# Kernel optimization log

Hardware: AMD Instinct MI355X
Metric: run time of the kernel (lower is better)

## Reference

```python
import jax, jax.numpy as jnp
import numpy as np

N = 100000      # nodes
E = 1200000     # edges (before self-loops)
DIN = 64        # n_input
DH = 64         # n_hidden
DOUT = 40       # n_output (classes)
L = 2           # n_layers
K = 4           # n_heads
ALPHA = 0.2
EPS = 1e-5


def setup_inputs() -> dict:
    key = jax.random.key(0)
    ks = jax.random.split(key, 12)
    s = lambda k, shape: jax.random.normal(k, shape, jnp.float32) * 0.05
    return {
        "x": jax.random.normal(ks[0], (N, DIN), jnp.float32),
        "edge_index": jax.random.randint(ks[1], (2, E), 0, N),
        # GCNConv weights: per layer l, per head k. conv_h: hidden->hidden, conv_x: input->hidden
        "Wh": s(ks[2], (L, K, DH, DH)), "bh": jnp.zeros((L, K, DH), jnp.float32),
        "Wx": s(ks[3], (L, K, DIN, DH)), "bx": jnp.zeros((L, K, DH), jnp.float32),
        # shared GatedModule
        "gf_w": s(ks[4], (2 * DH, 1)), "gf_b": jnp.zeros((1,), jnp.float32),
        "gu_w": s(ks[5], (2 * DH, 1)), "gu_b": jnp.zeros((1,), jnp.float32),
        # per-block FF
        "ff1_w": s(ks[6], (L, DH, DH)), "ff1_b": jnp.zeros((L, DH), jnp.float32),
        "ff2_w": s(ks[7], (L, DH, DH)), "ff2_b": jnp.zeros((L, DH), jnp.float32),
        # classifier head
        "clf1_w": s(ks[8], (DH, DH)), "clf1_b": jnp.zeros((DH,), jnp.float32),
        "clf2_w": s(ks[9], (DH, DOUT)), "clf2_b": jnp.zeros((DOUT,), jnp.float32),
    }


def _layer_norm(h):
    mu = jnp.mean(h, axis=-1, keepdims=True)
    var = jnp.mean((h - mu) ** 2, axis=-1, keepdims=True)
    return (h - mu) * jax.lax.rsqrt(var + EPS)


def reference(x, edge_index, Wh, bh, Wx, bx, gf_w, gf_b, gu_w, gu_b,
              ff1_w, ff1_b, ff2_w, ff2_b, clf1_w, clf1_b, clf2_w, clf2_b):
    # GCN normalization with self-loops: D^-1/2 (A+I) D^-1/2
    loops = jnp.arange(N)
    src = jnp.concatenate([edge_index[0], loops])  # [E+N]
    dst = jnp.concatenate([edge_index[1], loops])
    deg = jax.ops.segment_sum(jnp.ones_like(src, jnp.float32), dst, num_segments=N)
    dinv = jnp.where(deg > 0, jax.lax.rsqrt(jnp.maximum(deg, 1e-12)), 0.0)
    norm = dinv[src] * dinv[dst]  # [E+N] edge coefficients (shared by all convs)

    def gcn_conv(feat, W, b):
        m = feat @ W                                    # [N, DH] transform first (cheaper)
        agg = jax.ops.segment_sum(m[src] * norm[:, None], dst, num_segments=N)
        return agg + b

    def gate(h, xg):
        g = jnp.concatenate([h, xg], axis=1)            # [N, 2*DH]
        f = ALPHA * jnp.tanh(g @ gf_w + gf_b)
        u = ALPHA * jnp.tanh(g @ gu_w + gu_b)
        return (1.0 + f) * h + (1.0 + u) * xg

    h = jnp.zeros((N, DH), x.dtype)  # h0 = zeros (dropout is identity in eval mode)
    for l in range(L):
        acc = jnp.zeros((N, DH), x.dtype)
        for k in range(K):
            hk = gcn_conv(h, Wh[l, k], bh[l, k])
            xk = gcn_conv(x, Wx[l, k], bx[l, k])
            acc = acc + gate(hk, xk)
        h = acc / K + h                                  # multi-head mean + residual
        h = _layer_norm(h)
        ff = jax.nn.relu(h @ ff1_w[l] + ff1_b[l]) @ ff2_w[l] + ff2_b[l]
        h = _layer_norm(ff + h)
    return jax.nn.relu(h @ clf1_w + clf1_b) @ clf2_w + clf2_b
```

## Files before the change

### kernel.cpp

```cpp
#include <hip/hip_runtime.h>

#define NN 100000
#define EE 1200000
#define ALPHA_C 0.2f
#define EPS_C 1e-5f

typedef __attribute__((ext_vector_type(8))) short short8;
typedef __attribute__((ext_vector_type(4))) float f32x4;
#define MFMA __builtin_amdgcn_mfma_f32_16x16x32_bf16

#define PITCH 72


__device__ __forceinline__ ushort f2bf(float f) {
  unsigned u = __float_as_uint(f);
  unsigned r = (u + 0x7FFFu + ((u >> 16) & 1u)) >> 16;
  return (ushort)r;
}
__device__ __forceinline__ float bf2f(ushort h) { return __uint_as_float((unsigned)h << 16); }


__global__ __launch_bounds__(256) void k_zero2(int* __restrict__ a, int* __restrict__ b) {
  int i = blockIdx.x * 256 + threadIdx.x;
  if (i < NN) { a[i] = 0; b[i] = 0; }
}

__global__ __launch_bounds__(256) void k_count(const int* __restrict__ dstv, int* __restrict__ deg) {
  int e = blockIdx.x * 256 + threadIdx.x;
  if (e < EE) atomicAdd(&deg[dstv[e]], 1);
}

__global__ __launch_bounds__(256) void k_scan1(const int* __restrict__ deg, int* __restrict__ rowp,
                                               int* __restrict__ bsum, float* __restrict__ dinv) {
  __shared__ int s[256];
  int t = threadIdx.x;
  int i = blockIdx.x * 256 + t;
  int v = (i < NN) ? deg[i] : 0;
  if (i < NN) dinv[i] = rsqrtf((float)v + 1.0f);
  s[t] = v;
  __syncthreads();
  for (int off = 1; off < 256; off <<= 1) {
    int add = (t >= off) ? s[t - off] : 0;
    __syncthreads();
    s[t] += add;
    __syncthreads();
  }
  if (i < NN) rowp[i] = s[t] - v;
  if (t == 255) bsum[blockIdx.x] = s[255];
}

__global__ __launch_bounds__(512) void k_scan2(int* __restrict__ bsum, int* __restrict__ rowp, int nb) {
  __shared__ int s[512];
  int t = threadIdx.x;
  int v = (t < nb) ? bsum[t] : 0;
  s[t] = v;
  __syncthreads();
  for (int off = 1; off < 512; off <<= 1) {
    int add = (t >= off) ? s[t - off] : 0;
    __syncthreads();
    s[t] += add;
    __syncthreads();
  }
  if (t < nb) bsum[t] = s[t] - v;
  if (t == 0) rowp[NN] = EE;
}

__global__ __launch_bounds__(256) void k_scan3(int* __restrict__ rowp, const int* __restrict__ bsum) {
  int i = blockIdx.x * 256 + threadIdx.x;
  if (i < NN) rowp[i] += bsum[blockIdx.x];
}

__global__ __launch_bounds__(256) void k_fill(const int* __restrict__ srcv, const int* __restrict__ dstv,
                                              const int* __restrict__ rowp, int* __restrict__ fill,
                                              int* __restrict__ col) {
  int e = blockIdx.x * 256 + threadIdx.x;
  if (e < EE) {
    int d = dstv[e];
    int pos = rowp[d] + atomicAdd(&fill[d], 1);
    col[pos] = srcv[e];
  }
}


__global__ __launch_bounds__(256) void k_prescale(const float* __restrict__ feat,
                                                  const float* __restrict__ dinv,
                                                  float* __restrict__ xs) {
  int idx = blockIdx.x * 256 + threadIdx.x;
  if (idx < NN * 16) {
    float4 v = ((const float4*)feat)[idx];
    float d = dinv[idx >> 4];
    v.x *= d; v.y *= d; v.z *= d; v.w *= d;
    ((float4*)xs)[idx] = v;
  }
}

__global__ __launch_bounds__(256) void k_spmm(const float4* __restrict__ xs4, const float* __restrict__ dinv,
                                              const int* __restrict__ rowp, const int* __restrict__ col,
                                              float4* __restrict__ out4) {
  int node = blockIdx.x * 16 + (threadIdx.x >> 4);
  int q = threadIdx.x & 15;
  if (node >= NN) return;
  int s = rowp[node], e = rowp[node + 1];
  float4 a0 = {0.f, 0.f, 0.f, 0.f}, a1 = a0, a2 = a0, a3 = a0;
  int j = s;
  for (; j + 4 <= e; j += 4) {
    int c0 = col[j], c1 = col[j + 1], c2 = col[j + 2], c3 = col[j + 3];
    float4 v0 = xs4[c0 * 16 + q];
    float4 v1 = xs4[c1 * 16 + q];
    float4 v2 = xs4[c2 * 16 + q];
    float4 v3 = xs4[c3 * 16 + q];
    a0 += v0; a1 += v1; a2 += v2; a3 += v3;
  }
  for (; j < e; ++j) a0 += xs4[col[j] * 16 + q];
  float4 sv = xs4[node * 16 + q];
  float d = dinv[node];
  float4 o;
  o.x = d * (a0.x + a1.x + a2.x + a3.x + sv.x);
  o.y = d * (a0.y + a1.y + a2.y + a3.y + sv.y);
  o.z = d * (a0.z + a1.z + a2.z + a3.z + sv.z);
  o.w = d * (a0.w + a1.w + a2.w + a3.w + sv.w);
  out4[node * 16 + q] = o;
}


__global__ __launch_bounds__(256) void k_pack(const float* __restrict__ Wh, const float* __restrict__ Wx,
                                              const float* __restrict__ ff1w, const float* __restrict__ ff2w,
                                              const float* __restrict__ c1w, const float* __restrict__ c2w,
                                              ushort* __restrict__ wpk) {
  int id = blockIdx.x;
  const float* src;
  int ncol = 64, vcol = 64;
  if (id < 8) src = Wx + id * 4096;
  else if (id < 16) src = Wh + (id - 8) * 4096;
  else if (id < 18) src = ff1w + (id - 16) * 4096;
  else if (id < 20) src = ff2w + (id - 18) * 4096;
  else if (id == 20) src = c1w;
  else { src = c2w; ncol = 40; vcol = 40; }
  ushort* dst = wpk + (size_t)id * 8192;
  for (int p = threadIdx.x; p < 512; p += 256) {
    int f = p >> 6, l = p & 63;
    int kh = f & 1, tc = f >> 1;
    int r0 = 32 * kh + 8 * (l >> 4), c = 16 * tc + (l & 15);
#pragma unroll
    for (int j = 0; j < 8; ++j) {
      float v = (c < vcol) ? src[(r0 + j) * ncol + c] : 0.f;
      ushort h = f2bf(v);
      dst[f * 512 + l * 8 + j] = h;
      dst[4096 + f * 512 + l * 8 + j] = f2bf(v - bf2f(h));
    }
  }
}


__device__ __forceinline__ float red16(float v) {
  v += __shfl_xor(v, 1);
  v += __shfl_xor(v, 2);
  v += __shfl_xor(v, 4);
  v += __shfl_xor(v, 8);
  return v;
}

__device__ __forceinline__ void stage_tile(const float* __restrict__ src, int gbase,
                                           ushort* __restrict__ hi, ushort* __restrict__ lo, int t) {
#pragma unroll
  for (int u = 0; u < 4; ++u) {
    int f = u * 256 + t;
    int row = f >> 4, c4 = (f & 15) << 2;
    int gr = gbase + row;
    if (gr > NN - 1) gr = NN - 1;
    float4 v = *(const float4*)(src + gr * 64 + c4);
    ushort h0 = f2bf(v.x), h1 = f2bf(v.y), h2 = f2bf(v.z), h3 = f2bf(v.w);
    ushort l0 = f2bf(v.x - bf2f(h0)), l1 = f2bf(v.y - bf2f(h1)),
           l2 = f2bf(v.z - bf2f(h2)), l3 = f2bf(v.w - bf2f(h3));
    int o = row * PITCH + c4;
    *(ushort4*)(hi + o) = make_ushort4(h0, h1, h2, h3);
    *(ushort4*)(lo + o) = make_ushort4(l0, l1, l2, l3);
  }
}

__device__ __forceinline__ void stageB(const ushort* __restrict__ wp, ushort* __restrict__ bsta, int t) {
#pragma unroll
  for (int u = 0; u < 4; ++u) {
    int o = (u * 256 + t) * 8;
    *(short8*)(bsta + o) = *(const short8*)(wp + o);
  }
}

template <int NT>
__device__ __forceinline__ void mm_mfma_l(short8 a0h, short8 a1h, short8 a0l, short8 a1l,
                                          const ushort* __restrict__ bsta, int l, f32x4* C) {
#pragma unroll
  for (int tc = 0; tc < NT; ++tc) {
#pragma unroll
    for (int kh = 0; kh < 2; ++kh) {
      const short8 bh = *(const short8*)(bsta + (tc * 2 + kh) * 512 + l * 8);
      const short8 bl = *(const short8*)(bsta + 4096 + (tc * 2 + kh) * 512 + l * 8);
      const short8 ah = kh ? a1h : a0h;
      const short8 alo = kh ? a1l : a0l;
      C[tc] = MFMA(ah, bh, C[tc], 0, 0, 0);
      C[tc] = MFMA(ah, bl, C[tc], 0, 0, 0);
      C[tc] = MFMA(alo, bh, C[tc], 0, 0, 0);
    }
  }
}

__device__ __forceinline__ void ln_frag(float v[4][4]) {
#pragma unroll
  for (int r = 0; r < 4; ++r) {
    float s = v[0][r] + v[1][r] + v[2][r] + v[3][r];
    s = red16(s);
    float mu = s * 0.015625f;
    float q = 0.f;
#pragma unroll
    for (int tc = 0; tc < 4; ++tc) { float d = v[tc][r] - mu; q = fmaf(d, d, q); }
    q = red16(q);
    float inv = rsqrtf(q * 0.015625f + EPS_C);
#pragma unroll
    for (int tc = 0; tc < 4; ++tc) v[tc][r] = (v[tc][r] - mu) * inv;
  }
}


template <int HAS_H, int WSC>
__global__ __launch_bounds__(256) void k_layer(
    const float* __restrict__ aggX, const float* __restrict__ aggH,
    const float* __restrict__ h_in, float* __restrict__ h_out,
    float* __restrict__ hs_out, const float* __restrict__ dinv,
    const ushort* __restrict__ wxp, const ushort* __restrict__ whp,
    const float* __restrict__ bxl, const float* __restrict__ bhl,
    const float* __restrict__ gfw, const float* __restrict__ gfb,
    const float* __restrict__ guw, const float* __restrict__ gub,
    const ushort* __restrict__ ff1p, const float* __restrict__ ff1b,
    const ushort* __restrict__ ff2p, const float* __restrict__ ff2b) {
  __shared__ __align__(16) ushort th[64 * PITCH], tl[64 * PITCH];
  __shared__ __align__(16) ushort bsta[8192];
  const int t = threadIdx.x, blk = blockIdx.x;
  const int w = t >> 6, l = t & 63, lg = l >> 4, lr = l & 15;
  const int abase = (16 * w + lr) * PITCH + 8 * lg;

  stage_tile(aggX, blk * 64, th, tl, t);
  __syncthreads();
  short8 xa0h = *(const short8*)(th + abase);
  short8 xa1h = *(const short8*)(th + abase + 32);
  short8 xa0l = *(const short8*)(tl + abase);
  short8 xa1l = *(const short8*)(tl + abase + 32);
  short8 ha0h = (short8)0, ha1h = (short8)0, ha0l = (short8)0, ha1l = (short8)0;
  if (HAS_H) {
    __syncthreads();
    stage_tile(aggH, blk * 64, th, tl, t);
    __syncthreads();
    ha0h = *(const short8*)(th + abase);
    ha1h = *(const short8*)(th + abase + 32);
    ha0l = *(const short8*)(tl + abase);
    ha1l = *(const short8*)(tl + abase + 32);
  }

  float gfhw[4], gfxw[4], guhw[4], guxw[4];
#pragma unroll
  for (int tc = 0; tc < 4; ++tc) {
    gfhw[tc] = gfw[lr + 16 * tc]; gfxw[tc] = gfw[64 + lr + 16 * tc];
    guhw[tc] = guw[lr + 16 * tc]; guxw[tc] = guw[64 + lr + 16 * tc];
  }
  const float gfb0 = gfb[0], gub0 = gub[0];

  float acc[4][4];
#pragma unroll
  for (int tc = 0; tc < 4; ++tc)
#pragma unroll
    for (int r = 0; r < 4; ++r) acc[tc][r] = 0.f;

  for (int k = 0; k < 4; ++k) {
    f32x4 cx[4], ch[4];
#pragma unroll
    for (int tc = 0; tc < 4; ++tc) { cx[tc] = (f32x4)0.f; ch[tc] = (f32x4)0.f; }
    __syncthreads();
    stageB(wxp + k * 8192, bsta, t);
    __syncthreads();
    mm_mfma_l<4>(xa0h, xa1h, xa0l, xa1l, bsta, l, cx);
    if (HAS_H) {
      __syncthreads();
      stageB(whp + k * 8192, bsta, t);
      __syncthreads();
      mm_mfma_l<4>(ha0h, ha1h, ha0l, ha1l, bsta, l, ch);
    }

    float Cx[4][4], Ch[4][4];
#pragma unroll
    for (int tc = 0; tc < 4; ++tc) {
      float bxv = bxl[k * 64 + lr + 16 * tc];
      float bhv = bhl[k * 64 + lr + 16 * tc];
#pragma unroll
      for (int r = 0; r < 4; ++r) {
        Cx[tc][r] = cx[tc][r] + bxv;
        Ch[tc][r] = (HAS_H ? ch[tc][r] : 0.f) + bhv;
      }
    }
#pragma unroll
    for (int r = 0; r < 4; ++r) {
      float pf = 0.f, pu = 0.f;
#pragma unroll
      for (int tc = 0; tc < 4; ++tc) {
        pf = fmaf(Ch[tc][r], gfhw[tc], pf); pf = fmaf(Cx[tc][r], gfxw[tc], pf);
        pu = fmaf(Ch[tc][r], guhw[tc], pu); pu = fmaf(Cx[tc][r], guxw[tc], pu);
      }
      pf = red16(pf); pu = red16(pu);
      float fv = ALPHA_C * tanhf(pf + gfb0);
      float uv = ALPHA_C * tanhf(pu + gub0);
#pragma unroll
      for (int tc = 0; tc < 4; ++tc)
        acc[tc][r] += (1.f + fv) * Ch[tc][r] + (1.f + uv) * Cx[tc][r];
    }
  }

  float hmid[4][4];
#pragma unroll
  for (int tc = 0; tc < 4; ++tc)
#pragma unroll
    for (int r = 0; r < 4; ++r) {
      float hv = 0.f;
      if (HAS_H) {
        int gn = blk * 64 + 16 * w + 4 * lg + r;
        if (gn > NN - 1) gn = NN - 1;
        hv = h_in[gn * 64 + lr + 16 * tc];
      }
      hmid[tc][r] = fmaf(acc[tc][r], 0.25f, hv);
    }
  ln_frag(hmid);

  __syncthreads();
#pragma unroll
  for (int tc = 0; tc < 4; ++tc)
#pragma unroll
    for (int r = 0; r < 4; ++r) {
      int o = (16 * w + 4 * lg + r) * PITCH + lr + 16 * tc;
      ushort h = f2bf(hmid[tc][r]);
      th[o] = h;
      tl[o] = f2bf(hmid[tc][r] - bf2f(h));
    }
  __syncthreads();
  short8 m0h = *(const short8*)(th + abase);
  short8 m1h = *(const short8*)(th + abase + 32);
  short8 m0l = *(const short8*)(tl + abase);
  short8 m1l = *(const short8*)(tl + abase + 32);

  f32x4 f1[4];
#pragma unroll
  for (int tc = 0; tc < 4; ++tc) f1[tc] = (f32x4)0.f;
  __syncthreads();
  stageB(ff1p, bsta, t);
  __syncthreads();
  mm_mfma_l<4>(m0h, m1h, m0l, m1l, bsta, l, f1);
#pragma unroll
  for (int tc = 0; tc < 4; ++tc) {
    float bv = ff1b[lr + 16 * tc];
#pragma unroll
    for (int r = 0; r < 4; ++r) {
      float v = fmaxf(f1[tc][r] + bv, 0.f);
      int o = (16 * w + 4 * lg + r) * PITCH + lr + 16 * tc;
      ushort h = f2bf(v);
      th[o] = h;
      tl[o] = f2bf(v - bf2f(h));
    }
  }
  __syncthreads();
  short8 g0h = *(const short8*)(th + abase);
  short8 g1h = *(const short8*)(th + abase + 32);
  short8 g0l = *(const short8*)(tl + abase);
  short8 g1l = *(const short8*)(tl + abase + 32);

  f32x4 f2[4];
#pragma unroll
  for (int tc = 0; tc < 4; ++tc) f2[tc] = (f32x4)0.f;
  __syncthreads();
  stageB(ff2p, bsta, t);
  __syncthreads();
  mm_mfma_l<4>(g0h, g1h, g0l, g1l, bsta, l, f2);
  float F2[4][4];
#pragma unroll
  for (int tc = 0; tc < 4; ++tc) {
    float bv = ff2b[lr + 16 * tc];
#pragma unroll
    for (int r = 0; r < 4; ++r) F2[tc][r] = f2[tc][r] + bv + hmid[tc][r];
  }
  ln_frag(F2);

#pragma unroll
  for (int r = 0; r < 4; ++r) {
    int gn = blk * 64 + 16 * w + 4 * lg + r;
    if (gn < NN) {
      float dv = WSC ? dinv[gn] : 0.f;
#pragma unroll
      for (int tc = 0; tc < 4; ++tc) {
        h_out[gn * 64 + lr + 16 * tc] = F2[tc][r];
        if (WSC) hs_out[gn * 64 + lr + 16 * tc] = F2[tc][r] * dv;
      }
    }
  }
}


__global__ __launch_bounds__(256) void k_clf(const float* __restrict__ h,
                                             const ushort* __restrict__ c1p, const float* __restrict__ b1,
                                             const ushort* __restrict__ c2p, const float* __restrict__ b2,
                                             float* __restrict__ outv) {
  __shared__ __align__(16) ushort th[64 * PITCH], tl[64 * PITCH];
  __shared__ __align__(16) ushort bsta[8192];
  const int t = threadIdx.x, blk = blockIdx.x;
  const int w = t >> 6, l = t & 63, lg = l >> 4, lr = l & 15;
  const int abase = (16 * w + lr) * PITCH + 8 * lg;

  stage_tile(h, blk * 64, th, tl, t);
  __syncthreads();
  short8 a0h = *(const short8*)(th + abase);
  short8 a1h = *(const short8*)(th + abase + 32);
  short8 a0l = *(const short8*)(tl + abase);
  short8 a1l = *(const short8*)(tl + abase + 32);

  f32x4 c1[4];
#pragma unroll
  for (int tc = 0; tc < 4; ++tc) c1[tc] = (f32x4)0.f;
  stageB(c1p, bsta, t);
  __syncthreads();
  mm_mfma_l<4>(a0h, a1h, a0l, a1l, bsta, l, c1);
  __syncthreads();
#pragma unroll
  for (int tc = 0; tc < 4; ++tc) {
    float bv = b1[lr + 16 * tc];
#pragma unroll
    for (int r = 0; r < 4; ++r) {
      float v = fmaxf(c1[tc][r] + bv, 0.f);
      int o = (16 * w + 4 * lg + r) * PITCH + lr + 16 * tc;
      ushort hh = f2bf(v);
      th[o] = hh;
      tl[o] = f2bf(v - bf2f(hh));
    }
  }
  stageB(c2p, bsta, t);
  __syncthreads();
  short8 m0h = *(const short8*)(th + abase);
  short8 m1h = *(const short8*)(th + abase + 32);
  short8 m0l = *(const short8*)(tl + abase);
  short8 m1l = *(const short8*)(tl + abase + 32);

  f32x4 c2[3];
#pragma unroll
  for (int tc = 0; tc < 3; ++tc) c2[tc] = (f32x4)0.f;
  mm_mfma_l<3>(m0h, m1h, m0l, m1l, bsta, l, c2);
#pragma unroll
  for (int tc = 0; tc < 3; ++tc) {
    int cc = lr + 16 * tc;
    if (cc < 40) {
      float bv = b2[cc];
#pragma unroll
      for (int r = 0; r < 4; ++r) {
        int gn = blk * 64 + 16 * w + 4 * lg + r;
        if (gn < NN) outv[gn * 40 + cc] = c2[tc][r] + bv;
      }
    }
  }
}


extern "C" void kernel_launch(void* const* d_in, const int* in_sizes, int n_in,
                              void* d_out, int out_size, void* d_ws, size_t ws_size,
                              hipStream_t stream) {
  (void)in_sizes; (void)n_in; (void)out_size; (void)ws_size;
  const float* x    = (const float*)d_in[0];
  const int*   ei   = (const int*)d_in[1];
  const float* Wh   = (const float*)d_in[2];
  const float* bh   = (const float*)d_in[3];
  const float* Wx   = (const float*)d_in[4];
  const float* bx   = (const float*)d_in[5];
  const float* gfw  = (const float*)d_in[6];
  const float* gfb  = (const float*)d_in[7];
  const float* guw  = (const float*)d_in[8];
  const float* gub  = (const float*)d_in[9];
  const float* ff1w = (const float*)d_in[10];
  const float* ff1b = (const float*)d_in[11];
  const float* ff2w = (const float*)d_in[12];
  const float* ff2b = (const float*)d_in[13];
  const float* c1w  = (const float*)d_in[14];
  const float* c1b  = (const float*)d_in[15];
  const float* c2w  = (const float*)d_in[16];
  const float* c2b  = (const float*)d_in[17];
  float* outv = (float*)d_out;

  char* ws = (char*)d_ws;
  size_t o = 0;
  auto take = [&](size_t b) { char* p = ws + o; o += (b + 255) & ~(size_t)255; return p; };
  int*    deg  = (int*)take((size_t)NN * 4);
  int*    fill = (int*)take((size_t)NN * 4);
  int*    rowp = (int*)take((size_t)(NN + 1) * 4);
  int*    bsum = (int*)take(512 * 4);
  int*    col  = (int*)take((size_t)EE * 4);
  float*  dinv = (float*)take((size_t)NN * 4);
  ushort* wpk  = (ushort*)take((size_t)22 * 8192 * 2);
  float*  aggX = (float*)take((size_t)NN * 64 * 4);
  float*  aggH = (float*)take((size_t)NN * 64 * 4);
  float*  hbuf = (float*)take((size_t)NN * 64 * 4);
  float*  xsc  = (float*)take((size_t)NN * 64 * 4);

  const int* srcv = ei;
  const int* dstv = ei + EE;

  const int NB_E = (EE + 255) / 256;
  const int NB_N = (NN + 255) / 256;
  const int NB_V4 = (NN * 16 + 255) / 256;

  k_pack<<<22, 256, 0, stream>>>(Wh, Wx, ff1w, ff2w, c1w, c2w, wpk);
  k_zero2<<<NB_N, 256, 0, stream>>>(deg, fill);
  k_count<<<NB_E, 256, 0, stream>>>(dstv, deg);
  k_scan1<<<NB_N, 256, 0, stream>>>(deg, rowp, bsum, dinv);
  k_scan2<<<1, 512, 0, stream>>>(bsum, rowp, NB_N);
  k_scan3<<<NB_N, 256, 0, stream>>>(rowp, bsum);
  k_fill<<<NB_E, 256, 0, stream>>>(srcv, dstv, rowp, fill, col);

  k_prescale<<<NB_V4, 256, 0, stream>>>(x, dinv, xsc);
  k_spmm<<<(NN + 15) / 16, 256, 0, stream>>>((const float4*)xsc, dinv, rowp, col, (float4*)aggX);

  const int NB_L = (NN + 63) / 64;
  k_layer<0, 1><<<NB_L, 256, 0, stream>>>(
      aggX, aggX, hbuf, hbuf, xsc, dinv,
      wpk + 0 * 8192, wpk + 8 * 8192, bx, bh, gfw, gfb, guw, gub,
      wpk + 16 * 8192, ff1b, wpk + 18 * 8192, ff2b);

  k_spmm<<<(NN + 15) / 16, 256, 0, stream>>>((const float4*)xsc, dinv, rowp, col, (float4*)aggH);

  k_layer<1, 0><<<NB_L, 256, 0, stream>>>(
      aggX, aggH, hbuf, hbuf, xsc, dinv,
      wpk + 4 * 8192, wpk + 12 * 8192, bx + 256, bh + 256, gfw, gfb, guw, gub,
      wpk + 17 * 8192, ff1b + 64, wpk + 19 * 8192, ff2b + 64);

  k_clf<<<NB_L, 256, 0, stream>>>(hbuf, wpk + 20 * 8192, c1b, wpk + 21 * 8192, c2b, outv);
}
```

Before: 388.9 us.

## Double-buffer weight tiles with async global-to-LDS loads and use fast tanh

Replaces the synchronous register-staged weight copies in the layer kernel with a two-slot LDS buffer filled by global_load_lds. The next weight tile (next head, then ff1/ff2) is prefetched while the current MFMA runs, which removes several barriers per head. It also hoists the bias loads out of the head loop, fully unrolls that loop, and replaces tanhf with an exp-based approximation. The cost is more LDS per block, which may lower occupancy, and the ordering of the async LDS writes now relies on the remaining barriers being correct.

Result: slower. 398.1 us (+2.4%).

```diff
diff --git a/kernel.cpp b/kernel.cpp
--- a/kernel.cpp
+++ b/kernel.cpp
@@ -11,6 +11,9 @@
 
 #define PITCH 72
 
+typedef const __attribute__((address_space(1))) unsigned int* gas_t;
+typedef __attribute__((address_space(3))) unsigned int* las_t;
+
 
 __device__ __forceinline__ ushort f2bf(float f) {
   unsigned u = __float_as_uint(f);
@@ -18,6 +21,13 @@
   return (ushort)r;
 }
 __device__ __forceinline__ float bf2f(ushort h) { return __uint_as_float((unsigned)h << 16); }
+
+__device__ __forceinline__ float ftanh(float x) {
+  float ax = fabsf(x);
+  float e = __expf(2.f * ax);
+  float t = 1.f - 2.f / (e + 1.f);
+  return copysignf(t, x);
+}
 
 
 __global__ __launch_bounds__(256) void k_zero2(int* __restrict__ a, int* __restrict__ b) {
@@ -178,6 +188,18 @@
   }
 }
 
+__device__ __forceinline__ void issueB(const ushort* __restrict__ wp, ushort* buf, int t) {
+  const int lane = t & 63, w = t >> 6;
+  const char* g = (const char*)wp;
+  char* b = (char*)buf;
+  const int wo = w * 4096;
+#pragma unroll
+  for (int u = 0; u < 4; ++u) {
+    __builtin_amdgcn_global_load_lds((gas_t)(g + wo + u * 1024 + lane * 16),
+                                     (las_t)(b + wo + u * 1024), 16, 0, 0);
+  }
+}
+
 __device__ __forceinline__ void stageB(const ushort* __restrict__ wp, ushort* __restrict__ bsta, int t) {
 #pragma unroll
   for (int u = 0; u < 4; ++u) {
@@ -233,10 +255,12 @@
     const ushort* __restrict__ ff1p, const float* __restrict__ ff1b,
     const ushort* __restrict__ ff2p, const float* __restrict__ ff2b) {
   __shared__ __align__(16) ushort th[64 * PITCH], tl[64 * PITCH];
-  __shared__ __align__(16) ushort bsta[8192];
+  __shared__ __align__(16) ushort bsta[2][8192];
   const int t = threadIdx.x, blk = blockIdx.x;
   const int w = t >> 6, l = t & 63, lg = l >> 4, lr = l & 15;
   const int abase = (16 * w + lr) * PITCH + 8 * lg;
+
+  issueB(wxp, bsta[0], t);
 
   stage_tile(aggX, blk * 64, th, tl, t);
   __syncthreads();
@@ -256,10 +280,16 @@
   }
 
   float gfhw[4], gfxw[4], guhw[4], guxw[4];
+  float bxv[4][4], bhv[4][4];
 #pragma unroll
   for (int tc = 0; tc < 4; ++tc) {
     gfhw[tc] = gfw[lr + 16 * tc]; gfxw[tc] = gfw[64 + lr + 16 * tc];
     guhw[tc] = guw[lr + 16 * tc]; guxw[tc] = guw[64 + lr + 16 * tc];
+#pragma unroll
+    for (int k = 0; k < 4; ++k) {
+      bxv[k][tc] = bxl[k * 64 + lr + 16 * tc];
+      bhv[k][tc] = bhl[k * 64 + lr + 16 * tc];
+    }
   }
   const float gfb0 = gfb[0], gub0 = gub[0];
 
@@ -269,32 +299,31 @@
 #pragma unroll
     for (int r = 0; r < 4; ++r) acc[tc][r] = 0.f;
 
+#pragma unroll
   for (int k = 0; k < 4; ++k) {
     f32x4 cx[4], ch[4];
 #pragma unroll
     for (int tc = 0; tc < 4; ++tc) { cx[tc] = (f32x4)0.f; ch[tc] = (f32x4)0.f; }
-    __syncthreads();
-    stageB(wxp + k * 8192, bsta, t);
-    __syncthreads();
-    mm_mfma_l<4>(xa0h, xa1h, xa0l, xa1l, bsta, l, cx);
+
     if (HAS_H) {
+      issueB(whp + k * 8192, bsta[1], t);
+      mm_mfma_l<4>(xa0h, xa1h, xa0l, xa1l, bsta[0], l, cx);
       __syncthreads();
-      stageB(whp + k * 8192, bsta, t);
-      __syncthreads();
-      mm_mfma_l<4>(ha0h, ha1h, ha0l, ha1l, bsta, l, ch);
+      issueB(k < 3 ? (wxp + (k + 1) * 8192) : ff1p, bsta[0], t);
+      mm_mfma_l<4>(ha0h, ha1h, ha0l, ha1l, bsta[1], l, ch);
+    } else {
+      issueB(k < 3 ? (wxp + (k + 1) * 8192) : ff1p, bsta[(k + 1) & 1], t);
+      mm_mfma_l<4>(xa0h, xa1h, xa0l, xa1l, bsta[k & 1], l, cx);
     }
 
     float Cx[4][4], Ch[4][4];
 #pragma unroll
-    for (int tc = 0; tc < 4; ++tc) {
-      float bxv = bxl[k * 64 + lr + 16 * tc];
-      float bhv = bhl[k * 64 + lr + 16 * tc];
+    for (int tc = 0; tc < 4; ++tc)
 #pragma unroll
       for (int r = 0; r < 4; ++r) {
-        Cx[tc][r] = cx[tc][r] + bxv;
-        Ch[tc][r] = (HAS_H ? ch[tc][r] : 0.f) + bhv;
+        Cx[tc][r] = cx[tc][r] + bxv[k][tc];
+        Ch[tc][r] = (HAS_H ? ch[tc][r] : 0.f) + bhv[k][tc];
       }
-    }
 #pragma unroll
     for (int r = 0; r < 4; ++r) {
       float pf = 0.f, pu = 0.f;
@@ -304,12 +333,13 @@
         pu = fmaf(Ch[tc][r], guhw[tc], pu); pu = fmaf(Cx[tc][r], guxw[tc], pu);
       }
       pf = red16(pf); pu = red16(pu);
-      float fv = ALPHA_C * tanhf(pf + gfb0);
-      float uv = ALPHA_C * tanhf(pu + gub0);
+      float fv = ALPHA_C * ftanh(pf + gfb0);
+      float uv = ALPHA_C * ftanh(pu + gub0);
 #pragma unroll
       for (int tc = 0; tc < 4; ++tc)
         acc[tc][r] += (1.f + fv) * Ch[tc][r] + (1.f + uv) * Cx[tc][r];
     }
+    __syncthreads();
   }
 
   float hmid[4][4];
@@ -327,7 +357,7 @@
     }
   ln_frag(hmid);
 
-  __syncthreads();
+  issueB(ff2p, bsta[1], t);
 #pragma unroll
   for (int tc = 0; tc < 4; ++tc)
 #pragma unroll
@@ -346,22 +376,24 @@
   f32x4 f1[4];
 #pragma unroll
   for (int tc = 0; tc < 4; ++tc) f1[tc] = (f32x4)0.f;
-  __syncthreads();
-  stageB(ff1p, bsta, t);
-  __syncthreads();
-  mm_mfma_l<4>(m0h, m1h, m0l, m1l, bsta, l, f1);
+  mm_mfma_l<4>(m0h, m1h, m0l, m1l, bsta[0], l, f1);
+  float F1[4][4];
 #pragma unroll
   for (int tc = 0; tc < 4; ++tc) {
     float bv = ff1b[lr + 16 * tc];
 #pragma unroll
+    for (int r = 0; r < 4; ++r) F1[tc][r] = fmaxf(f1[tc][r] + bv, 0.f);
+  }
+  __syncthreads();
+#pragma unroll
+  for (int tc = 0; tc < 4; ++tc)
+#pragma unroll
     for (int r = 0; r < 4; ++r) {
-      float v = fmaxf(f1[tc][r] + bv, 0.f);
       int o = (16 * w + 4 * lg + r) * PITCH + lr + 16 * tc;
-      ushort h = f2bf(v);
+      ushort h = f2bf(F1[tc][r]);
       th[o] = h;
-      tl[o] = f2bf(v - bf2f(h));
-    }
-  }
+      tl[o] = f2bf(F1[tc][r] - bf2f(h));
+    }
   __syncthreads();
   short8 g0h = *(const short8*)(th + abase);
   short8 g1h = *(const short8*)(th + abase + 32);
@@ -371,10 +403,7 @@
   f32x4 f2[4];
 #pragma unroll
   for (int tc = 0; tc < 4; ++tc) f2[tc] = (f32x4)0.f;
-  __syncthreads();
-  stageB(ff2p, bsta, t);
-  __syncthreads();
-  mm_mfma_l<4>(g0h, g1h, g0l, g1l, bsta, l, f2);
+  mm_mfma_l<4>(g0h, g1h, g0l, g1l, bsta[1], l, f2);
   float F2[4][4];
 #pragma unroll
   for (int tc = 0; tc < 4; ++tc) {
```

## Fuse classifier into last layer kernel, merge zeroing into pack, fast tanh

Applied to the files above, without the earlier changes.

The classifier MLP now runs inside the second layer kernel on the register-resident normalized features, so the final hidden state is no longer written to global memory and read back by a separate kernel. The buffer-zeroing kernel is merged into the weight-packing kernel to save one launch. tanhf is replaced with an exp-based approximation in the gate. This removes about 25.6 MB of round-trip traffic and two launches, at the cost of a longer last-layer kernel and slightly different tanh rounding.

Result: faster. 380.9 us (-2.1%).

```diff
diff --git a/kernel.cpp b/kernel.cpp
--- a/kernel.cpp
+++ b/kernel.cpp
@@ -19,11 +19,13 @@
 }
 __device__ __forceinline__ float bf2f(ushort h) { return __uint_as_float((unsigned)h << 16); }
 
-
-__global__ __launch_bounds__(256) void k_zero2(int* __restrict__ a, int* __restrict__ b) {
-  int i = blockIdx.x * 256 + threadIdx.x;
-  if (i < NN) { a[i] = 0; b[i] = 0; }
-}
+__device__ __forceinline__ float ftanh(float x) {
+  float ax = fabsf(x);
+  float e = __expf(2.f * ax);
+  float t = 1.f - 2.f / (e + 1.f);
+  return copysignf(t, x);
+}
+
 
 __global__ __launch_bounds__(256) void k_count(const int* __restrict__ dstv, int* __restrict__ deg) {
   int e = blockIdx.x * 256 + threadIdx.x;
@@ -123,11 +125,15 @@
 }
 
 
-__global__ __launch_bounds__(256) void k_pack(const float* __restrict__ Wh, const float* __restrict__ Wx,
-                                              const float* __restrict__ ff1w, const float* __restrict__ ff2w,
-                                              const float* __restrict__ c1w, const float* __restrict__ c2w,
-                                              ushort* __restrict__ wpk) {
+__global__ __launch_bounds__(256) void k_packz(const float* __restrict__ Wh, const float* __restrict__ Wx,
+                                               const float* __restrict__ ff1w, const float* __restrict__ ff2w,
+                                               const float* __restrict__ c1w, const float* __restrict__ c2w,
+                                               ushort* __restrict__ wpk,
+                                               int* __restrict__ deg, int* __restrict__ fill) {
+  int i = blockIdx.x * 256 + threadIdx.x;
+  if (i < NN) { deg[i] = 0; fill[i] = 0; }
   int id = blockIdx.x;
+  if (id >= 22) return;
   const float* src;
   int ncol = 64, vcol = 64;
   if (id < 8) src = Wx + id * 4096;
@@ -221,7 +227,7 @@
 }
 
 
-template <int HAS_H, int WSC>
+template <int HAS_H, int WSC, int DO_CLF>
 __global__ __launch_bounds__(256) void k_layer(
     const float* __restrict__ aggX, const float* __restrict__ aggH,
     const float* __restrict__ h_in, float* __restrict__ h_out,
@@ -231,7 +237,10 @@
     const float* __restrict__ gfw, const float* __restrict__ gfb,
     const float* __restrict__ guw, const float* __restrict__ gub,
     const ushort* __restrict__ ff1p, const float* __restrict__ ff1b,
-    const ushort* __restrict__ ff2p, const float* __restrict__ ff2b) {
+    const ushort* __restrict__ ff2p, const float* __restrict__ ff2b,
+    const ushort* __restrict__ c1p, const float* __restrict__ c1b,
+    const ushort* __restrict__ c2p, const float* __restrict__ c2b,
+    float* __restrict__ outv) {
   __shared__ __align__(16) ushort th[64 * PITCH], tl[64 * PITCH];
   __shared__ __align__(16) ushort bsta[8192];
   const int t = threadIdx.x, blk = blockIdx.x;
@@ -304,8 +313,8 @@
         pu = fmaf(Ch[tc][r], guhw[tc], pu); pu = fmaf(Cx[tc][r], guxw[tc], pu);
       }
       pf = red16(pf); pu = red16(pu);
-      float fv = ALPHA_C * tanhf(pf + gfb0);
-      float uv = ALPHA_C * tanhf(pu + gub0);
+      float fv = ALPHA_C * ftanh(pf + gfb0);
+      float uv = ALPHA_C * ftanh(pu + gub0);
 #pragma unroll
       for (int tc = 0; tc < 4; ++tc)
         acc[tc][r] += (1.f + fv) * Ch[tc][r] + (1.f + uv) * Cx[tc][r];
@@ -384,48 +393,47 @@
   }
   ln_frag(F2);
 
-#pragma unroll
-  for (int r = 0; r < 4; ++r) {
-    int gn = blk * 64 + 16 * w + 4 * lg + r;
-    if (gn < NN) {
-      float dv = WSC ? dinv[gn] : 0.f;
-#pragma unroll
-      for (int tc = 0; tc < 4; ++tc) {
-        h_out[gn * 64 + lr + 16 * tc] = F2[tc][r];
-        if (WSC) hs_out[gn * 64 + lr + 16 * tc] = F2[tc][r] * dv;
+  if (!DO_CLF) {
+#pragma unroll
+    for (int r = 0; r < 4; ++r) {
+      int gn = blk * 64 + 16 * w + 4 * lg + r;
+      if (gn < NN) {
+        float dv = WSC ? dinv[gn] : 0.f;
+#pragma unroll
+        for (int tc = 0; tc < 4; ++tc) {
+          h_out[gn * 64 + lr + 16 * tc] = F2[tc][r];
+          if (WSC) hs_out[gn * 64 + lr + 16 * tc] = F2[tc][r] * dv;
+        }
       }
     }
-  }
-}
-
-
-__global__ __launch_bounds__(256) void k_clf(const float* __restrict__ h,
-                                             const ushort* __restrict__ c1p, const float* __restrict__ b1,
-                                             const ushort* __restrict__ c2p, const float* __restrict__ b2,
-                                             float* __restrict__ outv) {
-  __shared__ __align__(16) ushort th[64 * PITCH], tl[64 * PITCH];
-  __shared__ __align__(16) ushort bsta[8192];
-  const int t = threadIdx.x, blk = blockIdx.x;
-  const int w = t >> 6, l = t & 63, lg = l >> 4, lr = l & 15;
-  const int abase = (16 * w + lr) * PITCH + 8 * lg;
-
-  stage_tile(h, blk * 64, th, tl, t);
-  __syncthreads();
-  short8 a0h = *(const short8*)(th + abase);
-  short8 a1h = *(const short8*)(th + abase + 32);
-  short8 a0l = *(const short8*)(tl + abase);
-  short8 a1l = *(const short8*)(tl + abase + 32);
+    return;
+  }
+
+  __syncthreads();
+#pragma unroll
+  for (int tc = 0; tc < 4; ++tc)
+#pragma unroll
+    for (int r = 0; r < 4; ++r) {
+      int o = (16 * w + 4 * lg + r) * PITCH + lr + 16 * tc;
+      ushort h = f2bf(F2[tc][r]);
+      th[o] = h;
+      tl[o] = f2bf(F2[tc][r] - bf2f(h));
+    }
+  stageB(c1p, bsta, t);
+  __syncthreads();
+  short8 p0h = *(const short8*)(th + abase);
+  short8 p1h = *(const short8*)(th + abase + 32);
+  short8 p0l = *(const short8*)(tl + abase);
+  short8 p1l = *(const short8*)(tl + abase + 32);
 
   f32x4 c1[4];
 #pragma unroll
   for (int tc = 0; tc < 4; ++tc) c1[tc] = (f32x4)0.f;
-  stageB(c1p, bsta, t);
-  __syncthreads();
-  mm_mfma_l<4>(a0h, a1h, a0l, a1l, bsta, l, c1);
+  mm_mfma_l<4>(p0h, p1h, p0l, p1l, bsta, l, c1);
   __syncthreads();
 #pragma unroll
   for (int tc = 0; tc < 4; ++tc) {
-    float bv = b1[lr + 16 * tc];
+    float bv = c1b[lr + 16 * tc];
 #pragma unroll
     for (int r = 0; r < 4; ++r) {
       float v = fmaxf(c1[tc][r] + bv, 0.f);
@@ -437,20 +445,20 @@
   }
   stageB(c2p, bsta, t);
   __syncthreads();
-  short8 m0h = *(const short8*)(th + abase);
-  short8 m1h = *(const short8*)(th + abase + 32);
-  short8 m0l = *(const short8*)(tl + abase);
-  short8 m1l = *(const short8*)(tl + abase + 32);
+  short8 q0h = *(const short8*)(th + abase);
+  short8 q1h = *(const short8*)(th + abase + 32);
+  short8 q0l = *(const short8*)(tl + abase);
+  short8 q1l = *(const short8*)(tl + abase + 32);
 
   f32x4 c2[3];
 #pragma unroll
   for (int tc = 0; tc < 3; ++tc) c2[tc] = (f32x4)0.f;
-  mm_mfma_l<3>(m0h, m1h, m0l, m1l, bsta, l, c2);
+  mm_mfma_l<3>(q0h, q1h, q0l, q1l, bsta, l, c2);
 #pragma unroll
   for (int tc = 0; tc < 3; ++tc) {
     int cc = lr + 16 * tc;
     if (cc < 40) {
-      float bv = b2[cc];
+      float bv = c2b[cc];
 #pragma unroll
       for (int r = 0; r < 4; ++r) {
         int gn = blk * 64 + 16 * w + 4 * lg + r;
@@ -507,8 +515,7 @@
   const int NB_N = (NN + 255) / 256;
   const int NB_V4 = (NN * 16 + 255) / 256;
 
-  k_pack<<<22, 256, 0, stream>>>(Wh, Wx, ff1w, ff2w, c1w, c2w, wpk);
-  k_zero2<<<NB_N, 256, 0, stream>>>(deg, fill);
+  k_packz<<<NB_N, 256, 0, stream>>>(Wh, Wx, ff1w, ff2w, c1w, c2w, wpk, deg, fill);
   k_count<<<NB_E, 256, 0, stream>>>(dstv, deg);
   k_scan1<<<NB_N, 256, 0, stream>>>(deg, rowp, bsum, dinv);
   k_scan2<<<1, 512, 0, stream>>>(bsum, rowp, NB_N);
@@ -519,17 +526,17 @@
   k_spmm<<<(NN + 15) / 16, 256, 0, stream>>>((const float4*)xsc, dinv, rowp, col, (float4*)aggX);
 
   const int NB_L = (NN + 63) / 64;
-  k_layer<0, 1><<<NB_L, 256, 0, stream>>>(
+  k_layer<0, 1, 0><<<NB_L, 256, 0, stream>>>(
       aggX, aggX, hbuf, hbuf, xsc, dinv,
       wpk + 0 * 8192, wpk + 8 * 8192, bx, bh, gfw, gfb, guw, gub,
-      wpk + 16 * 8192, ff1b, wpk + 18 * 8192, ff2b);
+      wpk + 16 * 8192, ff1b, wpk + 18 * 8192, ff2b,
+      wpk + 20 * 8192, c1b, wpk + 21 * 8192, c2b, outv);
 
   k_spmm<<<(NN + 15) / 16, 256, 0, stream>>>((const float4*)xsc, dinv, rowp, col, (float4*)aggH);
 
-  k_layer<1, 0><<<NB_L, 256, 0, stream>>>(
+  k_layer<1, 0, 1><<<NB_L, 256, 0, stream>>>(
       aggX, aggH, hbuf, hbuf, xsc, dinv,
       wpk + 4 * 8192, wpk + 12 * 8192, bx + 256, bh + 256, gfw, gfb, guw, gub,
-      wpk + 17 * 8192, ff1b + 64, wpk + 19 * 8192, ff2b + 64);
-
-  k_clf<<<NB_L, 256, 0, stream>>>(hbuf, wpk + 20 * 8192, c1b, wpk + 21 * 8192, c2b, outv);
-}
+      wpk + 17 * 8192, ff1b + 64, wpk + 19 * 8192, ff2b + 64,
+      wpk + 20 * 8192, c1b, wpk + 21 * 8192, c2b, outv);
+}
```
